# Performance work log

Hardware: AMD Instinct MI355X
Metric: run time of the kernel (lower is better)

Reference implementation:

```python
import jax, jax.numpy as jnp
import numpy as np


def setup_inputs() -> dict:
    key = jax.random.key(0)
    ks = jax.random.split(key, 7)
    B, T, n_in, n_out, init_sz = 128, 1024, 3, 256, 2
    # small scales keep the 1024-step ReLU recurrence bounded
    return {
        "inputs": jax.random.normal(ks[0], (B, T, n_in), jnp.float32),
        "W1": jax.random.normal(ks[1], (64, init_sz), jnp.float32) * 0.3,
        "b1": jax.random.normal(ks[2], (64,), jnp.float32) * 0.1,
        "W2": jax.random.normal(ks[3], (n_out, 64), jnp.float32) * 0.1,
        "b2": jax.random.normal(ks[4], (n_out,), jnp.float32) * 0.1,
        "W_ih": jax.random.normal(ks[5], (n_out, n_in), jnp.float32) * 0.1,
        "W_hh": jax.random.normal(ks[6], (n_out, n_out), jnp.float32) * 0.05,
    }


def reference(inputs, W1, b1, W2, b2, W_ih, W_hh):
    B = inputs.shape[0]
    # initial_state: p0(ones(B, initial_state_size)) -> [num_layers=1, B, n_out]
    ones_in = jnp.ones((B, W1.shape[1]), inputs.dtype)
    h0 = jax.nn.relu(ones_in @ W1.T + b1)
    h0 = jax.nn.relu(h0 @ W2.T + b2)  # [B, n_out]

    # ReLU RNN, bias=False, batch_first: h_t = relu(x_t W_ih^T + h_{t-1} W_hh^T)
    xs = jnp.swapaxes(inputs, 0, 1)  # [T, B, n_in]
    xproj = xs @ W_ih.T              # [T, B, n_out] precompute input projection

    def step(h, xp):
        h = jax.nn.relu(xp + h @ W_hh.T)
        return h, h

    _, hs = jax.lax.scan(step, h0, xproj)
    p = jnp.swapaxes(hs, 0, 1)  # [B, T, n_out]

    # dp = cdist(p, p)**2 per batch; corr = exp(-dp)
    sq = jnp.sum(p * p, axis=-1)                       # [B, T]
    gram = jnp.einsum("btd,bsd->bts", p, p)            # [B, T, T]
    dp = jnp.maximum(sq[:, :, None] + sq[:, None, :] - 2.0 * gram, 0.0)
    corr = jnp.exp(-dp)
    return corr, p
```

## Files before the change

### kernel.cpp

```cpp
#include <hip/hip_runtime.h>
#include <stdint.h>

#define T_LEN 1024
#define H 256
#define B_SZ 128

typedef __attribute__((ext_vector_type(8))) __bf16 bf16x8;
typedef __attribute__((ext_vector_type(4))) float f32x4;

__device__ __forceinline__ unsigned short f32_to_bf16_rne(float f) {
  union { float f; unsigned int u; } c{f};
  unsigned int r = 0x7FFFu + ((c.u >> 16) & 1u);
  c.u += r;
  return (unsigned short)(c.u >> 16);
}
__device__ __forceinline__ float bf16_to_f32(unsigned short h) {
  union { unsigned int u; float f; } c{(unsigned int)h << 16};
  return c.f;
}

template <int CTRL>
__device__ __forceinline__ float dpp_xor_add(float x) {
  int v = __builtin_amdgcn_update_dpp(0, __float_as_int(x), CTRL, 0xF, 0xF, true);
  return x + __int_as_float(v);
}

__device__ __forceinline__ float xor32_add(float x) {
#if __has_builtin(__builtin_amdgcn_permlane32_swap)
  const int xi = __float_as_int(x);
  auto r = __builtin_amdgcn_permlane32_swap(xi, xi, false, false);
  return __int_as_float((int)r[0]) + __int_as_float((int)r[1]);
#else
  return x + __shfl_xor(x, 32, 64);
#endif
}

__global__ void h0_kernel(const float* __restrict__ W1, const float* __restrict__ b1,
                          const float* __restrict__ W2, const float* __restrict__ b2,
                          float* __restrict__ h0) {
  __shared__ float hid[64];
  const int tid = threadIdx.x;
  if (tid < 64) hid[tid] = fmaxf(W1[tid * 2 + 0] + W1[tid * 2 + 1] + b1[tid], 0.0f);
  __syncthreads();
  float acc = b2[tid];
  #pragma unroll
  for (int j = 0; j < 64; ++j) acc = fmaf(W2[tid * 64 + j], hid[j], acc);
  h0[tid] = fmaxf(acc, 0.0f);
}

__global__ __launch_bounds__(512, 2) void rnn_kernel(
    const float* __restrict__ inputs, const float* __restrict__ W_ih,
    const float* __restrict__ W_hh, const float* __restrict__ h0,
    float* __restrict__ p_out) {
  __shared__ float hbuf[2][H];
  const int b = blockIdx.x;
  const int tid = threadIdx.x;
  const int lane = tid & 63;
  const int w = tid >> 6;
  const int qlow = lane & 3;
  const int q2 = lane >> 5;
  const int q = qlow | (q2 << 2);
  const int g = (lane >> 2) & 7;

  float4 wv0[8], wv1[8], wv2[8], wv3[8];
  {
    const float* Wq = W_hh + (size_t)q * 32;
    const float4* r0 = reinterpret_cast<const float4*>(Wq + (size_t)(w * 32 + g +  0) * H);
    const float4* r1 = reinterpret_cast<const float4*>(Wq + (size_t)(w * 32 + g +  8) * H);
    const float4* r2 = reinterpret_cast<const float4*>(Wq + (size_t)(w * 32 + g + 16) * H);
    const float4* r3 = reinterpret_cast<const float4*>(Wq + (size_t)(w * 32 + g + 24) * H);
    #pragma unroll
    for (int j = 0; j < 8; ++j) {
      wv0[j] = r0[j]; wv1[j] = r1[j]; wv2[j] = r2[j]; wv3[j] = r3[j];
    }
  }

  int hidx[8];
  #pragma unroll
  for (int j = 0; j < 8; ++j) hidx[j] = (q << 3) | (j ^ q);

  const int duty = w * 32 + g + 8 * qlow;
  const int jd = (duty >> 2) & 7;
  const int dIdx = (w << 5) | ((jd ^ w) << 2) | (duty & 3);
  const float wih0 = W_ih[duty * 3 + 0];
  const float wih1 = W_ih[duty * 3 + 1];
  const float wih2 = W_ih[duty * 3 + 2];

  if (tid < H) {
    const int o = tid;
    const int jo = (o >> 2) & 7;
    const int qo = o >> 5;
    hbuf[0][(qo << 5) | ((jo ^ qo) << 2) | (o & 3)] = h0[o];
  }

  const float* xb = inputs + (size_t)b * T_LEN * 3;
  float* po = p_out + (size_t)b * T_LEN * H + duty;
  __syncthreads();

#define RNN_STEP(CUR, NXT, TT, X0, X1, X2)                                   \
  {                                                                          \
    const float4* h4 = reinterpret_cast<const float4*>(hbuf[CUR]);           \
    float a0 = 0.f, a1 = 0.f, a2 = 0.f, a3 = 0.f;                            \
    _Pragma("unroll") for (int j = 0; j < 8; ++j) {                          \
      const float4 hv = h4[hidx[j]];                                         \
      a0 = fmaf(wv0[j].x, hv.x, a0);                                         \
      a1 = fmaf(wv1[j].x, hv.x, a1);                                         \
      a2 = fmaf(wv2[j].x, hv.x, a2);                                         \
      a3 = fmaf(wv3[j].x, hv.x, a3);                                         \
      a0 = fmaf(wv0[j].y, hv.y, a0);                                         \
      a1 = fmaf(wv1[j].y, hv.y, a1);                                         \
      a2 = fmaf(wv2[j].y, hv.y, a2);                                         \
      a3 = fmaf(wv3[j].y, hv.y, a3);                                         \
      a0 = fmaf(wv0[j].z, hv.z, a0);                                         \
      a1 = fmaf(wv1[j].z, hv.z, a1);                                         \
      a2 = fmaf(wv2[j].z, hv.z, a2);                                         \
      a3 = fmaf(wv3[j].z, hv.z, a3);                                         \
      a0 = fmaf(wv0[j].w, hv.w, a0);                                         \
      a1 = fmaf(wv1[j].w, hv.w, a1);                                         \
      a2 = fmaf(wv2[j].w, hv.w, a2);                                         \
      a3 = fmaf(wv3[j].w, hv.w, a3);                                         \
    }                                                                        \
    a0 = dpp_xor_add<0xB1>(a0); a0 = dpp_xor_add<0x4E>(a0); a0 = xor32_add(a0); \
    a1 = dpp_xor_add<0xB1>(a1); a1 = dpp_xor_add<0x4E>(a1); a1 = xor32_add(a1); \
    a2 = dpp_xor_add<0xB1>(a2); a2 = dpp_xor_add<0x4E>(a2); a2 = xor32_add(a2); \
    a3 = dpp_xor_add<0xB1>(a3); a3 = dpp_xor_add<0x4E>(a3); a3 = xor32_add(a3); \
    const float tot = qlow == 0 ? a0 : qlow == 1 ? a1 : qlow == 2 ? a2 : a3; \
    float hn = fmaf((X2), wih2, fmaf((X1), wih1, fmaf((X0), wih0, tot)));    \
    hn = fmaxf(hn, 0.0f);                                                    \
    if (lane < 32) hbuf[NXT][dIdx] = hn;                                     \
    else           po[(size_t)(TT) * H] = hn;                                \
    asm volatile("s_waitcnt lgkmcnt(0)\n\ts_barrier" ::: "memory");          \
  }

  for (int t = 0; t < T_LEN; t += 2) {
    const float y0 = xb[t * 3 + 0];
    const float y1 = xb[t * 3 + 1];
    const float y2 = xb[t * 3 + 2];
    const float z0 = xb[t * 3 + 3];
    const float z1 = xb[t * 3 + 4];
    const float z2 = xb[t * 3 + 5];
    RNN_STEP(0, 1, t,     y0, y1, y2);
    RNN_STEP(1, 0, t + 1, z0, z1, z2);
  }
#undef RNN_STEP
}

__global__ void cvt_kernel(const float* __restrict__ p, unsigned short* __restrict__ pb,
                           float* __restrict__ sq) {
  const int gw = blockIdx.x * 4 + (threadIdx.x >> 6);
  const int lane = threadIdx.x & 63;
  const float4 v = reinterpret_cast<const float4*>(p + (size_t)gw * H)[lane];
  const unsigned short u0 = f32_to_bf16_rne(v.x);
  const unsigned short u1 = f32_to_bf16_rne(v.y);
  const unsigned short u2 = f32_to_bf16_rne(v.z);
  const unsigned short u3 = f32_to_bf16_rne(v.w);
  ushort4 st;
  st.x = u0; st.y = u1; st.z = u2; st.w = u3;
  reinterpret_cast<ushort4*>(pb + (size_t)gw * H)[lane] = st;
  const float r0 = bf16_to_f32(u0), r1 = bf16_to_f32(u1);
  const float r2 = bf16_to_f32(u2), r3 = bf16_to_f32(u3);
  float s = r0 * r0 + r1 * r1 + r2 * r2 + r3 * r3;
  #pragma unroll
  for (int off = 32; off > 0; off >>= 1) s += __shfl_down(s, off, 64);
  if (lane == 0) sq[gw] = s;
}

__global__ __launch_bounds__(256) void gram_kernel(
    const unsigned short* __restrict__ pb, const float* __restrict__ sq,
    float* __restrict__ corr) {
  __shared__ unsigned short At[128 * 64];
  __shared__ unsigned short Bt[128 * 64];
  __shared__ float sqT[128];
  __shared__ float sqS[128];

  const int b = blockIdx.y;
  const int t0 = (blockIdx.x >> 3) * 128;
  const int s0 = (blockIdx.x & 7) * 128;
  const int tid = threadIdx.x;

  if (tid < 128) sqT[tid] = sq[b * T_LEN + t0 + tid];
  else           sqS[tid - 128] = sq[b * T_LEN + s0 + (tid - 128)];

  const int lane = tid & 63;
  const int wave = tid >> 6;
  const int wm = wave >> 1;
  const int wn = wave & 1;
  const int m16 = lane & 15;
  const int kg = lane >> 4;

  f32x4 acc[4][4];
  #pragma unroll
  for (int i = 0; i < 4; ++i)
    #pragma unroll
    for (int j = 0; j < 4; ++j) acc[i][j] = (f32x4){0.f, 0.f, 0.f, 0.f};

  const size_t baseT = ((size_t)b * T_LEN + t0) * H;
  const size_t baseS = ((size_t)b * T_LEN + s0) * H;

  for (int kc = 0; kc < 4; ++kc) {
    #pragma unroll
    for (int i = 0; i < 4; ++i) {
      const int c = tid + 256 * i;
      const int r = c >> 3;
      const int k8 = c & 7;
      *reinterpret_cast<uint4*>(&At[r * 64 + k8 * 8]) =
          *reinterpret_cast<const uint4*>(pb + baseT + (size_t)r * H + kc * 64 + k8 * 8);
      *reinterpret_cast<uint4*>(&Bt[r * 64 + k8 * 8]) =
          *reinterpret_cast<const uint4*>(pb + baseS + (size_t)r * H + kc * 64 + k8 * 8);
    }
    __syncthreads();

    #pragma unroll
    for (int k32 = 0; k32 < 64; k32 += 32) {
      bf16x8 af[4], bfm[4];
      #pragma unroll
      for (int i = 0; i < 4; ++i)
        af[i] = *reinterpret_cast<const bf16x8*>(
            &At[(wm * 64 + i * 16 + m16) * 64 + k32 + kg * 8]);
      #pragma unroll
      for (int j = 0; j < 4; ++j)
        bfm[j] = *reinterpret_cast<const bf16x8*>(
            &Bt[(wn * 64 + j * 16 + m16) * 64 + k32 + kg * 8]);
      #pragma unroll
      for (int i = 0; i < 4; ++i)
        #pragma unroll
        for (int j = 0; j < 4; ++j)
          acc[i][j] = __builtin_amdgcn_mfma_f32_16x16x32_bf16(af[i], bfm[j], acc[i][j], 0, 0, 0);
    }
    __syncthreads();
  }

  #pragma unroll
  for (int i = 0; i < 4; ++i) {
    #pragma unroll
    for (int j = 0; j < 4; ++j) {
      #pragma unroll
      for (int r = 0; r < 4; ++r) {
        const int trow = wm * 64 + i * 16 + kg * 4 + r;
        const int scol = wn * 64 + j * 16 + m16;
        const float dp = fmaxf(sqT[trow] + sqS[scol] - 2.0f * acc[i][j][r], 0.0f);
        corr[((size_t)b * T_LEN + t0 + trow) * T_LEN + s0 + scol] = __expf(-dp);
      }
    }
  }
}

extern "C" void kernel_launch(void* const* d_in, const int* in_sizes, int n_in,
                              void* d_out, int out_size, void* d_ws, size_t ws_size,
                              hipStream_t stream) {
  const float* inputs = (const float*)d_in[0];
  const float* W1   = (const float*)d_in[1];
  const float* b1   = (const float*)d_in[2];
  const float* W2   = (const float*)d_in[3];
  const float* b2   = (const float*)d_in[4];
  const float* W_ih = (const float*)d_in[5];
  const float* W_hh = (const float*)d_in[6];

  float* corr = (float*)d_out;
  float* p = corr + (size_t)B_SZ * T_LEN * T_LEN;

  unsigned short* pb = (unsigned short*)d_ws;
  float* sq = (float*)((char*)d_ws + (size_t)B_SZ * T_LEN * H * 2);
  float* h0 = sq + (size_t)B_SZ * T_LEN;

  h0_kernel<<<1, 256, 0, stream>>>(W1, b1, W2, b2, h0);
  rnn_kernel<<<B_SZ, 512, 0, stream>>>(inputs, W_ih, W_hh, h0, p);
  cvt_kernel<<<B_SZ * T_LEN / 4, 256, 0, stream>>>(p, pb, sq);
  gram_kernel<<<dim3(64, B_SZ), 256, 0, stream>>>(pb, sq, corr);
}
```

Measured before the change: 1.458 ms.

## Exploit Gram symmetry, prefetch gram tiles, use packed FMA in RNN step

The gram kernel now launches only the upper-triangular 128x128 tile pairs (36 of 64) and writes each tile plus its transpose, removing nearly half of the MFMA work and global loads. It also prefetches the next K-chunk into registers while the current one is computed. The RNN inner product switches to 2-wide float vectors so the compiler can emit packed FMA, with two accumulator sets to shorten dependency chains. The cost is extra non-coalesced float4 transposed stores and some added register pressure.

```diff
diff --git a/kernel.cpp b/kernel.cpp
--- a/kernel.cpp
+++ b/kernel.cpp
@@ -7,6 +7,7 @@
 
 typedef __attribute__((ext_vector_type(8))) __bf16 bf16x8;
 typedef __attribute__((ext_vector_type(4))) float f32x4;
+typedef __attribute__((ext_vector_type(2))) float f32x2;
 
 __device__ __forceinline__ unsigned short f32_to_bf16_rne(float f) {
   union { float f; unsigned int u; } c{f};
@@ -62,17 +63,24 @@
   const int q = qlow | (q2 << 2);
   const int g = (lane >> 2) & 7;
 
-  float4 wv0[8], wv1[8], wv2[8], wv3[8];
+  f32x2 w0[16], w1[16], w2[16], w3[16];
   {
     const float* Wq = W_hh + (size_t)q * 32;
-    const float4* r0 = reinterpret_cast<const float4*>(Wq + (size_t)(w * 32 + g +  0) * H);
-    const float4* r1 = reinterpret_cast<const float4*>(Wq + (size_t)(w * 32 + g +  8) * H);
-    const float4* r2 = reinterpret_cast<const float4*>(Wq + (size_t)(w * 32 + g + 16) * H);
-    const float4* r3 = reinterpret_cast<const float4*>(Wq + (size_t)(w * 32 + g + 24) * H);
-    #pragma unroll
-    for (int j = 0; j < 8; ++j) {
-      wv0[j] = r0[j]; wv1[j] = r1[j]; wv2[j] = r2[j]; wv3[j] = r3[j];
+    const f32x2* r0 = reinterpret_cast<const f32x2*>(Wq + (size_t)(w * 32 + g +  0) * H);
+    const f32x2* r1 = reinterpret_cast<const f32x2*>(Wq + (size_t)(w * 32 + g +  8) * H);
+    const f32x2* r2 = reinterpret_cast<const f32x2*>(Wq + (size_t)(w * 32 + g + 16) * H);
+    const f32x2* r3 = reinterpret_cast<const f32x2*>(Wq + (size_t)(w * 32 + g + 24) * H);
+    #pragma unroll
+    for (int jj = 0; jj < 16; ++jj) {
+      w0[jj] = r0[jj]; w1[jj] = r1[jj]; w2[jj] = r2[jj]; w3[jj] = r3[jj];
     }
+  }
+  #pragma unroll
+  for (int jj = 0; jj < 16; ++jj) {
+    asm volatile("" : "+v"(w0[jj]));
+    asm volatile("" : "+v"(w1[jj]));
+    asm volatile("" : "+v"(w2[jj]));
+    asm volatile("" : "+v"(w3[jj]));
   }
 
   int hidx[8];
@@ -82,9 +90,10 @@
   const int duty = w * 32 + g + 8 * qlow;
   const int jd = (duty >> 2) & 7;
   const int dIdx = (w << 5) | ((jd ^ w) << 2) | (duty & 3);
-  const float wih0 = W_ih[duty * 3 + 0];
-  const float wih1 = W_ih[duty * 3 + 1];
-  const float wih2 = W_ih[duty * 3 + 2];
+  float wih0 = W_ih[duty * 3 + 0];
+  float wih1 = W_ih[duty * 3 + 1];
+  float wih2 = W_ih[duty * 3 + 2];
+  asm volatile("" : "+v"(wih0), "+v"(wih1), "+v"(wih2));
 
   if (tid < H) {
     const int o = tid;
@@ -100,26 +109,32 @@
 #define RNN_STEP(CUR, NXT, TT, X0, X1, X2)                                   \
   {                                                                          \
     const float4* h4 = reinterpret_cast<const float4*>(hbuf[CUR]);           \
-    float a0 = 0.f, a1 = 0.f, a2 = 0.f, a3 = 0.f;                            \
+    f32x2 acc[2][4];                                                         \
+    _Pragma("unroll") for (int pp = 0; pp < 2; ++pp)                         \
+      _Pragma("unroll") for (int oo = 0; oo < 4; ++oo)                       \
+        acc[pp][oo] = (f32x2){0.f, 0.f};                                     \
     _Pragma("unroll") for (int j = 0; j < 8; ++j) {                          \
       const float4 hv = h4[hidx[j]];                                         \
-      a0 = fmaf(wv0[j].x, hv.x, a0);                                         \
-      a1 = fmaf(wv1[j].x, hv.x, a1);                                         \
-      a2 = fmaf(wv2[j].x, hv.x, a2);                                         \
-      a3 = fmaf(wv3[j].x, hv.x, a3);                                         \
-      a0 = fmaf(wv0[j].y, hv.y, a0);                                         \
-      a1 = fmaf(wv1[j].y, hv.y, a1);                                         \
-      a2 = fmaf(wv2[j].y, hv.y, a2);                                         \
-      a3 = fmaf(wv3[j].y, hv.y, a3);                                         \
-      a0 = fmaf(wv0[j].z, hv.z, a0);                                         \
-      a1 = fmaf(wv1[j].z, hv.z, a1);                                         \
-      a2 = fmaf(wv2[j].z, hv.z, a2);                                         \
-      a3 = fmaf(wv3[j].z, hv.z, a3);                                         \
-      a0 = fmaf(wv0[j].w, hv.w, a0);                                         \
-      a1 = fmaf(wv1[j].w, hv.w, a1);                                         \
-      a2 = fmaf(wv2[j].w, hv.w, a2);                                         \
-      a3 = fmaf(wv3[j].w, hv.w, a3);                                         \
+      const f32x2 hlo = {hv.x, hv.y};                                        \
+      const f32x2 hhi = {hv.z, hv.w};                                        \
+      const int par = j & 1;                                                 \
+      acc[par][0] = __builtin_elementwise_fma(w0[2 * j], hlo, acc[par][0]);  \
+      acc[par][1] = __builtin_elementwise_fma(w1[2 * j], hlo, acc[par][1]);  \
+      acc[par][2] = __builtin_elementwise_fma(w2[2 * j], hlo, acc[par][2]);  \
+      acc[par][3] = __builtin_elementwise_fma(w3[2 * j], hlo, acc[par][3]);  \
+      acc[par][0] = __builtin_elementwise_fma(w0[2 * j + 1], hhi, acc[par][0]); \
+      acc[par][1] = __builtin_elementwise_fma(w1[2 * j + 1], hhi, acc[par][1]); \
+      acc[par][2] = __builtin_elementwise_fma(w2[2 * j + 1], hhi, acc[par][2]); \
+      acc[par][3] = __builtin_elementwise_fma(w3[2 * j + 1], hhi, acc[par][3]); \
     }                                                                        \
+    const f32x2 s0 = acc[0][0] + acc[1][0];                                  \
+    const f32x2 s1 = acc[0][1] + acc[1][1];                                  \
+    const f32x2 s2 = acc[0][2] + acc[1][2];                                  \
+    const f32x2 s3 = acc[0][3] + acc[1][3];                                  \
+    float a0 = s0.x + s0.y;                                                  \
+    float a1 = s1.x + s1.y;                                                  \
+    float a2 = s2.x + s2.y;                                                  \
+    float a3 = s3.x + s3.y;                                                  \
     a0 = dpp_xor_add<0xB1>(a0); a0 = dpp_xor_add<0x4E>(a0); a0 = xor32_add(a0); \
     a1 = dpp_xor_add<0xB1>(a1); a1 = dpp_xor_add<0x4E>(a1); a1 = xor32_add(a1); \
     a2 = dpp_xor_add<0xB1>(a2); a2 = dpp_xor_add<0x4E>(a2); a2 = xor32_add(a2); \
@@ -174,8 +189,11 @@
   __shared__ float sqS[128];
 
   const int b = blockIdx.y;
-  const int t0 = (blockIdx.x >> 3) * 128;
-  const int s0 = (blockIdx.x & 7) * 128;
+  int ti = 0, rem = blockIdx.x;
+  while (rem >= 8 - ti) { rem -= 8 - ti; ++ti; }
+  const int si = ti + rem;
+  const int t0 = ti * 128;
+  const int s0 = si * 128;
   const int tid = threadIdx.x;
 
   if (tid < 128) sqT[tid] = sq[b * T_LEN + t0 + tid];
@@ -197,18 +215,26 @@
   const size_t baseT = ((size_t)b * T_LEN + t0) * H;
   const size_t baseS = ((size_t)b * T_LEN + s0) * H;
 
+  uint4 ra[4], rb[4];
+#define GRAM_LD(KC)                                                          \
+  { _Pragma("unroll") for (int i = 0; i < 4; ++i) {                          \
+      const int c = tid + 256 * i; const int r = c >> 3; const int k8 = c & 7; \
+      ra[i] = *reinterpret_cast<const uint4*>(pb + baseT + (size_t)r * H + (KC) * 64 + k8 * 8); \
+      rb[i] = *reinterpret_cast<const uint4*>(pb + baseS + (size_t)r * H + (KC) * 64 + k8 * 8); } }
+
+  GRAM_LD(0);
+  #pragma unroll
   for (int kc = 0; kc < 4; ++kc) {
     #pragma unroll
     for (int i = 0; i < 4; ++i) {
       const int c = tid + 256 * i;
       const int r = c >> 3;
       const int k8 = c & 7;
-      *reinterpret_cast<uint4*>(&At[r * 64 + k8 * 8]) =
-          *reinterpret_cast<const uint4*>(pb + baseT + (size_t)r * H + kc * 64 + k8 * 8);
-      *reinterpret_cast<uint4*>(&Bt[r * 64 + k8 * 8]) =
-          *reinterpret_cast<const uint4*>(pb + baseS + (size_t)r * H + kc * 64 + k8 * 8);
+      *reinterpret_cast<uint4*>(&At[r * 64 + k8 * 8]) = ra[i];
+      *reinterpret_cast<uint4*>(&Bt[r * 64 + k8 * 8]) = rb[i];
     }
     __syncthreads();
+    if (kc < 3) GRAM_LD(kc + 1);
 
     #pragma unroll
     for (int k32 = 0; k32 < 64; k32 += 32) {
@@ -229,18 +255,25 @@
     }
     __syncthreads();
   }
+#undef GRAM_LD
 
   #pragma unroll
   for (int i = 0; i < 4; ++i) {
     #pragma unroll
     for (int j = 0; j < 4; ++j) {
+      const int trow0 = wm * 64 + i * 16 + kg * 4;
+      const int scol = wn * 64 + j * 16 + m16;
+      float ev[4];
       #pragma unroll
       for (int r = 0; r < 4; ++r) {
-        const int trow = wm * 64 + i * 16 + kg * 4 + r;
-        const int scol = wn * 64 + j * 16 + m16;
-        const float dp = fmaxf(sqT[trow] + sqS[scol] - 2.0f * acc[i][j][r], 0.0f);
-        corr[((size_t)b * T_LEN + t0 + trow) * T_LEN + s0 + scol] = __expf(-dp);
+        const float dp = fmaxf(sqT[trow0 + r] + sqS[scol] - 2.0f * acc[i][j][r], 0.0f);
+        ev[r] = __expf(-dp);
+        corr[((size_t)b * T_LEN + t0 + trow0 + r) * T_LEN + s0 + scol] = ev[r];
       }
+      float4 mv;
+      mv.x = ev[0]; mv.y = ev[1]; mv.z = ev[2]; mv.w = ev[3];
+      *reinterpret_cast<float4*>(
+          &corr[((size_t)b * T_LEN + s0 + scol) * T_LEN + t0 + trow0]) = mv;
     }
   }
 }
@@ -266,5 +299,5 @@
   h0_kernel<<<1, 256, 0, stream>>>(W1, b1, W2, b2, h0);
   rnn_kernel<<<B_SZ, 512, 0, stream>>>(inputs, W_ih, W_hh, h0, p);
   cvt_kernel<<<B_SZ * T_LEN / 4, 256, 0, stream>>>(p, pb, sq);
-  gram_kernel<<<dim3(64, B_SZ), 256, 0, stream>>>(pb, sq, corr);
-}
+  gram_kernel<<<dim3(36, B_SZ), 256, 0, stream>>>(pb, sq, corr);
+}
```

Result: slower. 1.525 ms (+4.6%).
